# Optimization experiments

Measured on AMD Instinct MI355X. Metric: run time of the kernel, lower is better.

The kernel has to match this reference:

```python
import jax, jax.numpy as jnp
import numpy as np
from jax import lax

C = 64      # mid_channels
CR = 16     # reduced channels (C // reduction_ratio 4)
G = 4       # groups (C // group_channels 16)
K = 7       # involution kernel size
L = 6       # number of involution layers (n_layers - 2)
EPS = 1e-5
DN = ('NCHW', 'OIHW', 'NCHW')


def conv3(x, w, b):
    # 3x3 conv, stride 1, no padding (torch Conv2d default)
    y = lax.conv_general_dilated(x, w, (1, 1), [(0, 0), (0, 0)], dimension_numbers=DN)
    return y + b[None, :, None, None]


def conv1x1(x, w, b):
    # pointwise conv as einsum over channels
    return jnp.einsum('oi,bihw->bohw', w, x) + b[None, :, None, None]


def involution(x, wr, br, g, bt, mu, var, ws, bs):
    B, Cc, H, W = x.shape
    # kernel generation: 1x1 reduce -> BN (eval) -> ReLU -> 1x1 span
    t = conv1x1(x, wr, br)
    t = (t - mu[None, :, None, None]) * (g * jax.lax.rsqrt(var + EPS))[None, :, None, None] + bt[None, :, None, None]
    t = jax.nn.relu(t)
    w = conv1x1(t, ws, bs)                    # (B, G*K*K, H, W)
    w = w.reshape(B, G, K * K, H, W)
    # unfold: patches ordered (C, Kh, Kw) along channel dim, matching torch unfold
    p = lax.conv_general_dilated_patches(x, (K, K), (1, 1), [(K // 2, K // 2)] * 2, dimension_numbers=DN)
    p = p.reshape(B, G, Cc // G, K * K, H, W)
    out = jnp.einsum('bgkhw,bgckhw->bgchw', w, p)
    return out.reshape(B, Cc, H, W)


def setup_inputs() -> dict:
    key = jax.random.key(0)
    ks = jax.random.split(key, 9)
    s = 0.05
    return {
        'input_tensor': jax.random.normal(ks[0], (1, 3, 128, 128), jnp.float32),
        'conv_in_w': jax.random.normal(ks[1], (C, 3, 3, 3), jnp.float32) * s,
        'conv_in_b': jax.random.normal(ks[2], (C,), jnp.float32) * s,
        'w_reduce': jax.random.normal(ks[3], (L, CR, C), jnp.float32) * s,
        'b_reduce': jax.random.normal(ks[4], (L, CR), jnp.float32) * s,
        'bn_gamma': jnp.ones((L, CR), jnp.float32),
        'bn_beta': jnp.zeros((L, CR), jnp.float32),
        'bn_mean': jnp.zeros((L, CR), jnp.float32),
        'bn_var': jnp.ones((L, CR), jnp.float32),
        'w_span': jax.random.normal(ks[5], (L, G * K * K, CR), jnp.float32) * s,
        'b_span': jax.random.normal(ks[6], (L, G * K * K), jnp.float32) * s,
        'conv_out_w': jax.random.normal(ks[7], (2 * C, C, 3, 3), jnp.float32) * s,
        'conv_out_b': jax.random.normal(ks[8], (2 * C,), jnp.float32) * s,
    }


def reference(input_tensor, conv_in_w, conv_in_b, w_reduce, b_reduce, bn_gamma,
              bn_beta, bn_mean, bn_var, w_span, b_span, conv_out_w, conv_out_b):
    x = conv3(input_tensor, conv_in_w, conv_in_b)          # (1, 64, 126, 126)
    for i in range(L):
        x = jax.nn.relu(involution(x, w_reduce[i], b_reduce[i], bn_gamma[i],
                                   bn_beta[i], bn_mean[i], bn_var[i],
                                   w_span[i], b_span[i]))
    return conv3(x, conv_out_w, conv_out_b)                # (1, 128, 124, 124)
```

## Files before the change

kernel.cpp:

```cpp
#include <hip/hip_runtime.h>

#define IH 126
#define IW 126
#define HW 15876
#define OH 124
#define OW 124
#define OHW 15376

__global__ __launch_bounds__(256) void conv_in_kernel(
    const float* __restrict__ x, const float* __restrict__ w,
    const float* __restrict__ b, float* __restrict__ y)
{
  int pix = blockIdx.x * 256 + threadIdx.x;
  if (pix >= HW) return;
  int oc = blockIdx.y;
  int h  = pix / IW;
  int wc = pix - h * IW;
  const float* wp = w + oc * 27;
  float acc = b[oc];
#pragma unroll
  for (int ci = 0; ci < 3; ci++)
#pragma unroll
    for (int ky = 0; ky < 3; ky++)
#pragma unroll
      for (int kx = 0; kx < 3; kx++)
        acc = fmaf(x[ci * 128 * 128 + (h + ky) * 128 + (wc + kx)],
                   wp[ci * 9 + ky * 3 + kx], acc);
  y[oc * HW + pix] = acc;
}

__global__ __launch_bounds__(512, 4) void inv_kernel(
    const float* __restrict__ x, float* __restrict__ y,
    const float* __restrict__ wr, const float* __restrict__ br,
    const float* __restrict__ gam, const float* __restrict__ bet,
    const float* __restrict__ mu, const float* __restrict__ var,
    const float* __restrict__ wspan, const float* __restrict__ bspan)
{
  __shared__ __align__(16) float xs[140][68];
  __shared__ __align__(16) float wvs[6272];
  __shared__ __align__(16) float tss[640];
  float* ob  = &xs[0][0];

  int tid = threadIdx.x;
  int bx = blockIdx.x & 15, by = blockIdx.x >> 4;
  int ox0 = bx * 8, oy0 = by * 4;
  int xh0 = ox0 - 3, yh0 = oy0 - 3;

  for (int idx = tid; idx < 140 * 64; idx += 512) {
    int c = idx / 140;
    int pos = idx - c * 140;
    int row = pos / 14;
    int col = pos - row * 14;
    int gy = yh0 + row, gx = xh0 + col;
    float v = 0.f;
    if (gy >= 0 && gy < IH && gx >= 0 && gx < IW)
      v = x[c * HW + gy * IW + gx];
    xs[pos][c] = v;
  }
  __syncthreads();

  int w_ = __builtin_amdgcn_readfirstlane(tid >> 6);
  int ln = tid & 63;
  int p  = ln & 31;
  int prow = p >> 3, pcol = p & 7;
  int pc = (prow + 3) * 14 + (pcol + 3);

  {
    int cr0 = 2 * w_;
    const float* wa = wr + cr0 * 64;
    const float* wb = wa + 64;
    float a0 = 0.f, a1 = 0.f;
#pragma unroll
    for (int ci = 0; ci < 64; ci += 4) {
      float4 xv = *(const float4*)&xs[pc][ci];
      a0 = fmaf(xv.x, wa[ci + 0], a0); a1 = fmaf(xv.x, wb[ci + 0], a1);
      a0 = fmaf(xv.y, wa[ci + 1], a0); a1 = fmaf(xv.y, wb[ci + 1], a1);
      a0 = fmaf(xv.z, wa[ci + 2], a0); a1 = fmaf(xv.z, wb[ci + 2], a1);
      a0 = fmaf(xv.w, wa[ci + 3], a0); a1 = fmaf(xv.w, wb[ci + 3], a1);
    }
    float s0 = gam[cr0]     * rsqrtf(var[cr0]     + 1e-5f);
    float s1 = gam[cr0 + 1] * rsqrtf(var[cr0 + 1] + 1e-5f);
    float t0 = (a0 + br[cr0]     - mu[cr0])     * s0 + bet[cr0];
    float t1 = (a1 + br[cr0 + 1] - mu[cr0 + 1]) * s1 + bet[cr0 + 1];
    if (ln < 32) {
      tss[p * 20 + cr0]     = fmaxf(t0, 0.f);
      tss[p * 20 + cr0 + 1] = fmaxf(t1, 0.f);
    }
  }
  __syncthreads();

  {
    float tv[16];
#pragma unroll
    for (int i = 0; i < 4; i++) {
      float4 t4 = *(const float4*)&tss[p * 20 + 4 * i];
      tv[4 * i] = t4.x; tv[4 * i + 1] = t4.y;
      tv[4 * i + 2] = t4.z; tv[4 * i + 3] = t4.w;
    }
    for (int j = 0; j < 25; j++) {
      int pair = w_ + 8 * j;
      if (pair < 196) {
        const float* wk = wspan + pair * 16;
        float a = bspan[pair];
#pragma unroll
        for (int i = 0; i < 16; i++) a = fmaf(tv[i], wk[i], a);
        if (ln < 32) wvs[pair * 32 + pcol * 4 + prow] = a;
      }
    }
  }
  __syncthreads();

  float acc0 = 0.f, acc1 = 0.f, acc2 = 0.f, acc3 = 0.f;
  {
    int c = ln;
    int g = ln >> 4;
    float xw[4][7];
#pragma unroll
    for (int r = 0; r < 4; r++)
#pragma unroll
      for (int kx = 0; kx < 7; kx++)
        xw[r][kx] = xs[r * 14 + w_ + kx][c];
#pragma unroll
    for (int ky = 0; ky < 7; ky++) {
      if (ky > 0) {
#pragma unroll
        for (int r = 0; r < 3; r++)
#pragma unroll
          for (int kx = 0; kx < 7; kx++) xw[r][kx] = xw[r + 1][kx];
#pragma unroll
        for (int kx = 0; kx < 7; kx++)
          xw[3][kx] = xs[(ky + 3) * 14 + w_ + kx][c];
      }
#pragma unroll
      for (int kx = 0; kx < 7; kx++) {
        int k = ky * 7 + kx;
        float4 w4 = *(const float4*)&wvs[(g * 49 + k) * 32 + w_ * 4];
        acc0 = fmaf(w4.x, xw[0][kx], acc0);
        acc1 = fmaf(w4.y, xw[1][kx], acc1);
        acc2 = fmaf(w4.z, xw[2][kx], acc2);
        acc3 = fmaf(w4.w, xw[3][kx], acc3);
      }
    }
  }
  __syncthreads();

  {
    int c = ln;
    ob[c * 33 + 0 * 8 + w_] = fmaxf(acc0, 0.f);
    ob[c * 33 + 1 * 8 + w_] = fmaxf(acc1, 0.f);
    ob[c * 33 + 2 * 8 + w_] = fmaxf(acc2, 0.f);
    ob[c * 33 + 3 * 8 + w_] = fmaxf(acc3, 0.f);
  }
  __syncthreads();
  for (int j = tid; j < 2048; j += 512) {
    int c2 = j >> 5, pp = j & 31;
    int pr = pp >> 3, pc2 = pp & 7;
    int gy = oy0 + pr, gx = ox0 + pc2;
    if (gy < IH && gx < IW)
      y[c2 * HW + gy * IW + gx] = ob[c2 * 33 + pp];
  }
}

__global__ __launch_bounds__(256) void transpose_w_kernel(
    const float* __restrict__ w, float* __restrict__ wt)
{
  int i = blockIdx.x * 256 + threadIdx.x;
  if (i >= 128 * 64 * 9) return;
  int oc = i / 576;
  int rem = i - oc * 576;
  int ci = rem / 9;
  int k = rem - ci * 9;
  wt[(k * 64 + ci) * 128 + oc] = w[i];
}

__global__ __launch_bounds__(256, 2) void conv_out_kernel(
    const float* __restrict__ x, const float* __restrict__ wt,
    const float* __restrict__ b, float* __restrict__ y)
{
  __shared__ __align__(16) float xsm[16 * 160 * 4];
  int tid = threadIdx.x;
  int bx = blockIdx.x & 15, by = blockIdx.x >> 4;
  int oy0 = by * 8, ox0 = bx * 8;

  for (int u = tid; u < 1600; u += 256) {
    int cq = u / 100;
    int pos = u - cq * 100;
    int r = pos / 10;
    int c = pos - r * 10;
    int gy = oy0 + r, gx = ox0 + c;
    float4 v = make_float4(0.f, 0.f, 0.f, 0.f);
    if (gy < IH && gx < IW) {
      const float* xp = x + cq * 4 * HW + gy * IW + gx;
      v.x = xp[0]; v.y = xp[HW]; v.z = xp[2 * HW]; v.w = xp[3 * HW];
    }
    *(float4*)&xsm[(cq * 160 + r * 16 + c) * 4] = v;
  }
  __syncthreads();

  int ln = tid & 63;
  int px = ln & 7, py = ln >> 3;
  int wv_ = __builtin_amdgcn_readfirstlane(tid >> 6);
  int oc16 = blockIdx.y * 64 + wv_ * 16;

  float acc[16];
#pragma unroll
  for (int j = 0; j < 16; j++) acc[j] = b[oc16 + j];

#pragma unroll
  for (int ky = 0; ky < 3; ky++) {
#pragma unroll
    for (int kx = 0; kx < 3; kx++) {
      int k = ky * 3 + kx;
      const float* wp = wt + k * 64 * 128 + oc16;
      const float* xbase = &xsm[((py + ky) * 16 + px + kx) * 4];
#pragma unroll 2
      for (int cq = 0; cq < 16; cq++) {
        float4 xv = *(const float4*)(xbase + cq * 640);
        const float* wq = wp + cq * 4 * 128;
#pragma unroll
        for (int j = 0; j < 16; j++) {
          acc[j] = fmaf(xv.x, wq[0 * 128 + j], acc[j]);
          acc[j] = fmaf(xv.y, wq[1 * 128 + j], acc[j]);
          acc[j] = fmaf(xv.z, wq[2 * 128 + j], acc[j]);
          acc[j] = fmaf(xv.w, wq[3 * 128 + j], acc[j]);
        }
      }
    }
  }

  int oy = oy0 + py, ox = ox0 + px;
  if (oy < OH && ox < OW) {
#pragma unroll
    for (int j = 0; j < 16; j++)
      y[(oc16 + j) * OHW + oy * OW + ox] = acc[j];
  }
}

extern "C" void kernel_launch(void* const* d_in, const int* in_sizes, int n_in,
                              void* d_out, int out_size, void* d_ws, size_t ws_size,
                              hipStream_t stream)
{
  const float* input = (const float*)d_in[0];
  const float* ciw   = (const float*)d_in[1];
  const float* cib   = (const float*)d_in[2];
  const float* wred  = (const float*)d_in[3];
  const float* bred  = (const float*)d_in[4];
  const float* gam   = (const float*)d_in[5];
  const float* bet   = (const float*)d_in[6];
  const float* mu    = (const float*)d_in[7];
  const float* var   = (const float*)d_in[8];
  const float* wspan = (const float*)d_in[9];
  const float* bspan = (const float*)d_in[10];
  const float* cow   = (const float*)d_in[11];
  const float* cob   = (const float*)d_in[12];
  float* out = (float*)d_out;

  float* bufA = (float*)d_ws;
  float* bufB = bufA + (1 << 20);
  float* wt   = bufA + (1 << 21);

  transpose_w_kernel<<<288, 256, 0, stream>>>(cow, wt);
  conv_in_kernel<<<dim3(63, 64), 256, 0, stream>>>(input, ciw, cib, bufA);

  float* cur = bufA; float* nxt = bufB;
  for (int i = 0; i < 6; i++) {
    inv_kernel<<<512, 512, 0, stream>>>(cur, nxt,
        wred + i * 16 * 64, bred + i * 16, gam + i * 16, bet + i * 16,
        mu + i * 16, var + i * 16, wspan + i * 196 * 16, bspan + i * 196);
    float* t = cur; cur = nxt; nxt = t;
  }
  conv_out_kernel<<<dim3(256, 2), 256, 0, stream>>>(cur, wt, cob, out);
}
```

Baseline: 263.2 us.

## Split conv_out work across waves by kernel tap with LDS reduction

The output conv now gives each block 16 output channels instead of 64 and launches 8 channel groups. Within a block, the four waves split the nine 3x3 taps among themselves and their partial sums are reduced through shared memory. The weight transpose uses a blocked layout so each wave reads 64 contiguous floats per channel quad. The shared tile shrinks and occupancy hints rise to 6 blocks per SM, giving more blocks and parallelism for the final conv. In exchange, the input tile is reloaded by four times as many blocks, the tap split is unbalanced (wave 0 does 3 taps, others 2), and an extra LDS reduction is added.

```diff
diff --git a/kernel.cpp b/kernel.cpp
--- a/kernel.cpp
+++ b/kernel.cpp
@@ -170,14 +170,15 @@
   int rem = i - oc * 576;
   int ci = rem / 9;
   int k = rem - ci * 9;
-  wt[(k * 64 + ci) * 128 + oc] = w[i];
-}
-
-__global__ __launch_bounds__(256, 2) void conv_out_kernel(
+  int idx = ((k * 16 + (ci >> 2)) * 8 + (oc >> 4)) * 64 + (ci & 3) * 16 + (oc & 15);
+  wt[idx] = w[i];
+}
+
+__global__ __launch_bounds__(256, 6) void conv_out_kernel(
     const float* __restrict__ x, const float* __restrict__ wt,
     const float* __restrict__ b, float* __restrict__ y)
 {
-  __shared__ __align__(16) float xsm[16 * 160 * 4];
+  __shared__ __align__(16) float xsm[16 * 100 * 4];
   int tid = threadIdx.x;
   int bx = blockIdx.x & 15, by = blockIdx.x >> 4;
   int oy0 = by * 8, ox0 = bx * 8;
@@ -193,46 +194,59 @@
       const float* xp = x + cq * 4 * HW + gy * IW + gx;
       v.x = xp[0]; v.y = xp[HW]; v.z = xp[2 * HW]; v.w = xp[3 * HW];
     }
-    *(float4*)&xsm[(cq * 160 + r * 16 + c) * 4] = v;
+    *(float4*)&xsm[u * 4] = v;
   }
   __syncthreads();
 
   int ln = tid & 63;
   int px = ln & 7, py = ln >> 3;
   int wv_ = __builtin_amdgcn_readfirstlane(tid >> 6);
-  int oc16 = blockIdx.y * 64 + wv_ * 16;
+  int oc16 = blockIdx.y * 16;
 
   float acc[16];
 #pragma unroll
-  for (int j = 0; j < 16; j++) acc[j] = b[oc16 + j];
-
-#pragma unroll
-  for (int ky = 0; ky < 3; ky++) {
-#pragma unroll
-    for (int kx = 0; kx < 3; kx++) {
-      int k = ky * 3 + kx;
-      const float* wp = wt + k * 64 * 128 + oc16;
-      const float* xbase = &xsm[((py + ky) * 16 + px + kx) * 4];
+  for (int j = 0; j < 16; j++) acc[j] = (wv_ == 0) ? b[oc16 + j] : 0.f;
+
+  for (int kk = wv_; kk < 9; kk += 4) {
+    int ky = kk / 3, kx = kk - ky * 3;
+    const float* wp = wt + ((kk * 16) * 8 + blockIdx.y) * 64;
+    const float* xbase = &xsm[((py + ky) * 10 + px + kx) * 4];
 #pragma unroll 2
-      for (int cq = 0; cq < 16; cq++) {
-        float4 xv = *(const float4*)(xbase + cq * 640);
-        const float* wq = wp + cq * 4 * 128;
-#pragma unroll
-        for (int j = 0; j < 16; j++) {
-          acc[j] = fmaf(xv.x, wq[0 * 128 + j], acc[j]);
-          acc[j] = fmaf(xv.y, wq[1 * 128 + j], acc[j]);
-          acc[j] = fmaf(xv.z, wq[2 * 128 + j], acc[j]);
-          acc[j] = fmaf(xv.w, wq[3 * 128 + j], acc[j]);
-        }
-      }
-    }
-  }
-
-  int oy = oy0 + py, ox = ox0 + px;
-  if (oy < OH && ox < OW) {
+    for (int cq = 0; cq < 16; cq++) {
+      float4 xv = *(const float4*)(xbase + cq * 400);
+      const float* wq = wp + cq * 512;
+#pragma unroll
+      for (int j = 0; j < 16; j++) {
+        acc[j] = fmaf(xv.x, wq[j],      acc[j]);
+        acc[j] = fmaf(xv.y, wq[16 + j], acc[j]);
+        acc[j] = fmaf(xv.z, wq[32 + j], acc[j]);
+        acc[j] = fmaf(xv.w, wq[48 + j], acc[j]);
+      }
+    }
+  }
+
+  __syncthreads();
+  if (wv_ > 0) {
+#pragma unroll
+    for (int j4 = 0; j4 < 4; j4++) {
+      float4 v = make_float4(acc[4 * j4], acc[4 * j4 + 1],
+                             acc[4 * j4 + 2], acc[4 * j4 + 3]);
+      *(float4*)&xsm[(((wv_ - 1) * 64 + ln) * 16 + 4 * j4)] = v;
+    }
+  }
+  __syncthreads();
+  if (wv_ == 0) {
 #pragma unroll
     for (int j = 0; j < 16; j++)
-      y[(oc16 + j) * OHW + oy * OW + ox] = acc[j];
+      acc[j] += xsm[(0 * 64 + ln) * 16 + j]
+              + xsm[(1 * 64 + ln) * 16 + j]
+              + xsm[(2 * 64 + ln) * 16 + j];
+    int oy = oy0 + py, ox = ox0 + px;
+    if (oy < OH && ox < OW) {
+#pragma unroll
+      for (int j = 0; j < 16; j++)
+        y[(oc16 + j) * OHW + oy * OW + ox] = acc[j];
+    }
   }
 }
 
@@ -269,5 +283,5 @@
         mu + i * 16, var + i * 16, wspan + i * 196 * 16, bspan + i * 196);
     float* t = cur; cur = nxt; nxt = t;
   }
-  conv_out_kernel<<<dim3(256, 2), 256, 0, stream>>>(cur, wt, cob, out);
-}
+  conv_out_kernel<<<dim3(256, 8), 256, 0, stream>>>(cur, wt, cob, out);
+}
```

After: 262.4 us. About the same (-0.3%).
